# Optimization experiments

Hardware: AMD Instinct MI355X
Metric: run time of the kernel (lower is better)

The kernel has to match this reference:

```python
import jax, jax.numpy as jnp
import numpy as np

N_NODES = 100000
N_EDGES = 1600000
NODE_DIM = 64
EDGE_DIM = 32
HIDDEN = 64
LN_EPS = 1e-5


def _leaky_relu(x):
    return jnp.where(x >= 0, x, 0.1 * x)


def setup_inputs() -> dict:
    key = jax.random.key(0)
    ks = jax.random.split(key, 12)
    inp = {
        "node_features": jax.random.normal(ks[0], (N_NODES, NODE_DIM), dtype=jnp.float32),
        "edge_index": jax.random.randint(ks[1], (2, N_EDGES), 0, N_NODES, dtype=jnp.int32),
        "edge_attr": jax.random.normal(ks[2], (N_EDGES, EDGE_DIM), dtype=jnp.float32),
        "edge_weights": jax.random.uniform(ks[3], (N_EDGES,), dtype=jnp.float32),
        # message_mlp: Linear(node+edge -> hidden), LeakyReLU(0.1), Linear(hidden -> node)
        "mW1": jax.random.normal(ks[4], (NODE_DIM + EDGE_DIM, HIDDEN), dtype=jnp.float32) * 0.1,
        "mb1": jnp.zeros((HIDDEN,), dtype=jnp.float32),
        "mW2": jax.random.normal(ks[5], (HIDDEN, NODE_DIM), dtype=jnp.float32) * 0.1,
        "mb2": jnp.zeros((NODE_DIM,), dtype=jnp.float32),
        # update_mlp: Linear(2*node -> hidden), LayerNorm(hidden), LeakyReLU(0.1), Linear(hidden -> node)
        "uW1": jax.random.normal(ks[6], (2 * NODE_DIM, HIDDEN), dtype=jnp.float32) * 0.1,
        "ub1": jnp.zeros((HIDDEN,), dtype=jnp.float32),
        "ln_g": jnp.ones((HIDDEN,), dtype=jnp.float32),
        "ln_b": jnp.zeros((HIDDEN,), dtype=jnp.float32),
        "uW2": jax.random.normal(ks[7], (HIDDEN, NODE_DIM), dtype=jnp.float32) * 0.1,
        "ub2": jnp.zeros((NODE_DIM,), dtype=jnp.float32),
    }
    return inp


def reference(node_features, edge_index, edge_attr, edge_weights,
              mW1, mb1, mW2, mb2, uW1, ub1, ln_g, ln_b, uW2, ub2):
    src_idx, dst_idx = edge_index[0], edge_index[1]
    src_features = node_features[src_idx]                    # [E, node_dim] gather
    msg_input = jnp.concatenate([src_features, edge_attr], axis=-1)  # [E, node+edge]
    h = _leaky_relu(msg_input @ mW1 + mb1)                    # [E, hidden]
    messages = (h @ mW2 + mb2) * edge_weights[:, None]        # [E, node_dim]
    aggregated = jax.ops.segment_sum(messages, dst_idx, num_segments=node_features.shape[0])
    combined = jnp.concatenate([node_features, aggregated], axis=-1)  # [N, 2*node_dim]
    z = combined @ uW1 + ub1                                  # [N, hidden]
    mu = jnp.mean(z, axis=-1, keepdims=True)
    var = jnp.mean((z - mu) ** 2, axis=-1, keepdims=True)
    z = (z - mu) * jax.lax.rsqrt(var + LN_EPS) * ln_g + ln_b
    z = _leaky_relu(z)
    return z @ uW2 + ub2                                      # [N, node_dim]
```

## Files before the change

kernel.cpp:

```cpp
#include <hip/hip_runtime.h>
#include <cstdint>
#include <cstddef>

#define NN 100000
#define NE 1600000

#define QSCALE 262144.0f
#define QINV   3.814697265625e-06f

typedef __attribute__((ext_vector_type(8))) short bf16x8;
typedef __attribute__((ext_vector_type(4))) short bf16x4;
typedef __attribute__((ext_vector_type(4))) float f32x4;

#define OFF_W    0u
#define OFF_CNT  45056u
#define OFF_OFF  445056u
#define OFF_CUR  845120u
#define OFF_BS   1245120u
#define OFF_SE   1245632u
#define OFF_SD   14045632u
#define WS_NEED  20445632u

__device__ __forceinline__ short f2bf(float f) {
  uint32_t u = __builtin_bit_cast(uint32_t, f);
  u += 0x7FFFu + ((u >> 16) & 1u);
  return (short)(u >> 16);
}

__device__ __forceinline__ float lrelu(float x) { return fmaxf(x, 0.1f * x); }

__device__ __forceinline__ void atomic_add_f32(float* p, float v) {
  __hip_atomic_fetch_add(p, v, __ATOMIC_RELAXED, __HIP_MEMORY_SCOPE_AGENT);
}

__global__ void prep_kernel(const float* __restrict__ W1, const float* __restrict__ W2,
                            const float* __restrict__ uW1, const float* __restrict__ uW2,
                            short* __restrict__ ws) {
  int t = blockIdx.x * 256 + threadIdx.x;
  const int n1 = 64 * 96, n2 = 64 * 64, n3 = 64 * 128, n4 = 64 * 64;
  if (t < n1) { int c = t / 96, k = t % 96; ws[t] = f2bf(W1[k * 64 + c]); return; }
  t -= n1;
  if (t < n2) { int c = t / 64, k = t % 64; ws[n1 + t] = f2bf(W2[k * 64 + c]); return; }
  t -= n2;
  if (t < n3) { int c = t / 128, k = t % 128; ws[n1 + n2 + t] = f2bf(uW1[k * 64 + c]); return; }
  t -= n3;
  if (t < n4) { int c = t / 64, k = t % 64; ws[n1 + n2 + n3 + t] = f2bf(uW2[k * 64 + c]); return; }
}

__global__ __launch_bounds__(256) void hist_kernel(const int* __restrict__ ei,
                                                   int* __restrict__ cnt) {
  int t = blockIdx.x * 256 + threadIdx.x;
  if (t < NE) atomicAdd(&cnt[ei[NE + t]], 1);
}

__global__ __launch_bounds__(1024) void scan_block_kernel(const int* __restrict__ cnt,
                                                          int* __restrict__ off,
                                                          int* __restrict__ bs) {
  __shared__ int wsum[16];
  const int tid = threadIdx.x, lane = tid & 63, w = tid >> 6;
  const int i = blockIdx.x * 1024 + tid;
  int v = (i < NN) ? cnt[i] : 0;
  int x = v;
#pragma unroll
  for (int d = 1; d < 64; d <<= 1) { int t = __shfl_up(x, d); if (lane >= d) x += t; }
  if (lane == 63) wsum[w] = x;
  __syncthreads();
  if (w == 0) {
    int s = (lane < 16) ? wsum[lane] : 0;
#pragma unroll
    for (int d = 1; d < 16; d <<= 1) { int t = __shfl_up(s, d); if (lane >= d) s += t; }
    if (lane < 16) wsum[lane] = s;
  }
  __syncthreads();
  int incl = x + ((w > 0) ? wsum[w - 1] : 0);
  if (i < NN) off[i] = incl - v;
  if (tid == 1023) bs[blockIdx.x] = incl;
}

__global__ __launch_bounds__(1024) void scan_add_kernel(int* __restrict__ off,
                                                        const int* __restrict__ bs,
                                                        int* __restrict__ cur) {
  __shared__ int sbase;
  const int tid = threadIdx.x, cB = blockIdx.x;
  if (tid < 64) {
    int s = 0;
    if (tid < cB && tid < 98) s += bs[tid];
    int j2 = tid + 64;
    if (j2 < cB && j2 < 98) s += bs[j2];
#pragma unroll
    for (int d = 1; d < 64; d <<= 1) s += __shfl_xor(s, d);
    if (tid == 0) sbase = s;
  }
  __syncthreads();
  const int base = sbase;
  const int i = cB * 1024 + tid;
  if (i < NN) { int o = off[i] + base; off[i] = o; cur[i] = o; }
}

__global__ __launch_bounds__(256) void scatter_kernel(const int* __restrict__ ei,
                                                      int* __restrict__ cur,
                                                      int2* __restrict__ sse,
                                                      int* __restrict__ sdst) {
  int t = blockIdx.x * 256 + threadIdx.x;
  if (t >= NE) return;
  int d = ei[NE + t];
  int pos = atomicAdd(&cur[d], 1);
  sse[pos] = make_int2(ei[t], t);
  sdst[pos] = d;
}

__global__ __launch_bounds__(128) void fused_kernel(
    const float* __restrict__ nf, const float* __restrict__ ea,
    const float* __restrict__ ew,
    const int2* __restrict__ sse, const int* __restrict__ sdst,
    const int* __restrict__ off,
    const short* __restrict__ W1t, const float* __restrict__ b1,
    const short* __restrict__ W2t, const float* __restrict__ b2,
    const short* __restrict__ uW1t, const float* __restrict__ ub1,
    const float* __restrict__ gam, const float* __restrict__ bet,
    const short* __restrict__ uW2t, const float* __restrict__ ub2,
    float* __restrict__ out) {
  __shared__ __align__(16) char hbuf[2][8192];
  __shared__ int   sAgg[32 * 65];
  __shared__ int   tdstS[2][64];
  __shared__ float twS[2][64];

  const int tid = threadIdx.x;
  const int wv = tid >> 6, ln = tid & 63;
  const int c = ln & 15, g = ln >> 4;
  char* hb = hbuf[wv];
  const int nb = blockIdx.x * 32;

  for (int i = tid; i < 32 * 65; i += 128) sAgg[i] = 0;

  const int e0 = off[nb];
  const int e1 = (nb + 32 >= NN) ? NE : off[nb + 32];
  __syncthreads();

  float b1v[4][4];
#pragma unroll
  for (int m = 0; m < 4; ++m)
#pragma unroll
    for (int r = 0; r < 4; ++r) b1v[m][r] = b1[16 * m + 4 * g + r];
  float b2v[4];
#pragma unroll
  for (int n = 0; n < 4; ++n) b2v[n] = b2[16 * n + c];

  int t0 = e0 + wv * 64;
  if (t0 < e1) {
    int msx, msy, md; float mw;
    {
      int slot = t0 + ln;
      int cl = (slot < e1) ? slot : (e1 - 1);
      int2 se = sse[cl];
      msx = se.x; msy = se.y; md = sdst[cl]; mw = ew[se.y];
    }

    for (; t0 < e1; t0 += 128) {
      {
        bool val = (t0 + ln) < e1;
        tdstS[wv][ln] = val ? (md - nb) : 0;
        twS[wv][ln]   = val ? mw : 0.f;
      }
      int src[4], eid[4];
#pragma unroll
      for (int n = 0; n < 4; ++n) {
        src[n] = __shfl(msx, 16 * n + c);
        eid[n] = __shfl(msy, 16 * n + c);
      }

      int nsx = msx, nsy = msy, nd = md; float nw = mw;
      if (t0 + 128 < e1) {
        int slot = t0 + 128 + ln;
        int cl = (slot < e1) ? slot : (e1 - 1);
        int2 se = sse[cl];
        nsx = se.x; nsy = se.y; nd = sdst[cl]; nw = ew[se.y];
      }

      f32x4 acc1[4][4];
#pragma unroll
      for (int i = 0; i < 4; ++i)
#pragma unroll
        for (int j = 0; j < 4; ++j) acc1[i][j] = f32x4{0.f, 0.f, 0.f, 0.f};

#pragma unroll
      for (int ks = 0; ks < 3; ++ks) {
        bf16x8 xf[4];
#pragma unroll
        for (int n = 0; n < 4; ++n) {
          const float* p = (ks < 2) ? (nf + (size_t)src[n] * 64 + ks * 32 + g * 8)
                                    : (ea + (size_t)eid[n] * 32 + g * 8);
          float4 u = *(const float4*)p;
          float4 v = *(const float4*)(p + 4);
          bf16x8 t;
          t[0] = f2bf(u.x); t[1] = f2bf(u.y); t[2] = f2bf(u.z); t[3] = f2bf(u.w);
          t[4] = f2bf(v.x); t[5] = f2bf(v.y); t[6] = f2bf(v.z); t[7] = f2bf(v.w);
          xf[n] = t;
        }
#pragma unroll
        for (int m = 0; m < 4; ++m) {
          bf16x8 wf = *(const bf16x8*)(W1t + (size_t)(16 * m + c) * 96 + ks * 32 + g * 8);
#pragma unroll
          for (int n = 0; n < 4; ++n)
            acc1[m][n] = __builtin_amdgcn_mfma_f32_16x16x32_bf16(wf, xf[n], acc1[m][n], 0, 0, 0);
        }
      }

#pragma unroll
      for (int m = 0; m < 4; ++m) {
        const int h0 = 16 * m + 4 * g;
#pragma unroll
        for (int n = 0; n < 4; ++n) {
          const int e = 16 * n + c;
          bf16x4 pk;
#pragma unroll
          for (int r = 0; r < 4; ++r) pk[r] = f2bf(lrelu(acc1[m][n][r] + b1v[m][r]));
          const int byte = e * 128 + ((h0 * 2) ^ ((e & 7) << 4));
          *(bf16x4*)(hb + byte) = pk;
        }
      }

      f32x4 acc2[4][4];
#pragma unroll
      for (int i = 0; i < 4; ++i)
#pragma unroll
        for (int j = 0; j < 4; ++j) acc2[i][j] = f32x4{0.f, 0.f, 0.f, 0.f};
#pragma unroll
      for (int ks = 0; ks < 2; ++ks) {
        bf16x8 hf[4];
#pragma unroll
        for (int m = 0; m < 4; ++m) {
          const int e = 16 * m + c;
          const int byte = e * 128 + ((ks * 64 + g * 16) ^ ((e & 7) << 4));
          hf[m] = *(const bf16x8*)(hb + byte);
        }
#pragma unroll
        for (int n = 0; n < 4; ++n) {
          bf16x8 wf = *(const bf16x8*)(W2t + (size_t)(16 * n + c) * 64 + ks * 32 + g * 8);
#pragma unroll
          for (int m = 0; m < 4; ++m)
            acc2[m][n] = __builtin_amdgcn_mfma_f32_16x16x32_bf16(hf[m], wf, acc2[m][n], 0, 0, 0);
        }
      }

#pragma unroll
      for (int m = 0; m < 4; ++m)
#pragma unroll
        for (int r = 0; r < 4; ++r) {
          const int el = 16 * m + 4 * g + r;
          const int dl = tdstS[wv][el];
          const float w = twS[wv][el];
#pragma unroll
          for (int n = 0; n < 4; ++n)
            atomicAdd(&sAgg[dl * 65 + 16 * n + c],
                      __float2int_rn((acc2[m][n][r] + b2v[n]) * w * QSCALE));
        }

      msx = nsx; msy = nsy; md = nd; mw = nw;
    }
  }
  __syncthreads();

  const int nodeN = nb + 16 * wv + c;

  f32x4 un[4];
#pragma unroll
  for (int m = 0; m < 4; ++m) un[m] = f32x4{0.f, 0.f, 0.f, 0.f};

#pragma unroll
  for (int ks = 0; ks < 4; ++ks) {
    bf16x8 xf;
    if (ks < 2) {
      const float* p = nf + (size_t)nodeN * 64 + ks * 32 + g * 8;
      float4 u = *(const float4*)p;
      float4 v = *(const float4*)(p + 4);
      xf[0] = f2bf(u.x); xf[1] = f2bf(u.y); xf[2] = f2bf(u.z); xf[3] = f2bf(u.w);
      xf[4] = f2bf(v.x); xf[5] = f2bf(v.y); xf[6] = f2bf(v.z); xf[7] = f2bf(v.w);
    } else {
      const int* p = sAgg + (16 * wv + c) * 65 + (ks - 2) * 32 + g * 8;
#pragma unroll
      for (int j = 0; j < 8; ++j) xf[j] = f2bf((float)p[j] * QINV);
    }
#pragma unroll
    for (int m = 0; m < 4; ++m) {
      bf16x8 wf = *(const bf16x8*)(uW1t + (size_t)(16 * m + c) * 128 + ks * 32 + g * 8);
      un[m] = __builtin_amdgcn_mfma_f32_16x16x32_bf16(wf, xf, un[m], 0, 0, 0);
    }
  }

  float b1n[4][4], gn[4][4], bn[4][4];
#pragma unroll
  for (int m = 0; m < 4; ++m)
#pragma unroll
    for (int r = 0; r < 4; ++r) {
      int h = 16 * m + 4 * g + r;
      b1n[m][r] = ub1[h]; gn[m][r] = gam[h]; bn[m][r] = bet[h];
    }

  float s = 0.f;
#pragma unroll
  for (int m = 0; m < 4; ++m)
#pragma unroll
    for (int r = 0; r < 4; ++r) { un[m][r] += b1n[m][r]; s += un[m][r]; }
  s += __shfl_xor(s, 16);
  s += __shfl_xor(s, 32);
  const float mu = s * 0.015625f;
  float vs = 0.f;
#pragma unroll
  for (int m = 0; m < 4; ++m)
#pragma unroll
    for (int r = 0; r < 4; ++r) { float d = un[m][r] - mu; vs += d * d; }
  vs += __shfl_xor(vs, 16);
  vs += __shfl_xor(vs, 32);
  const float rstd = rsqrtf(vs * 0.015625f + 1e-5f);

#pragma unroll
  for (int m = 0; m < 4; ++m) {
    bf16x4 pk;
#pragma unroll
    for (int r = 0; r < 4; ++r)
      pk[r] = f2bf(lrelu((un[m][r] - mu) * rstd * gn[m][r] + bn[m][r]));
    const int byte = c * 128 + (((16 * m + 4 * g) * 2) ^ ((c & 7) << 4));
    *(bf16x4*)(hb + byte) = pk;
  }

  f32x4 ac[4];
#pragma unroll
  for (int n = 0; n < 4; ++n) ac[n] = f32x4{0.f, 0.f, 0.f, 0.f};
#pragma unroll
  for (int ks = 0; ks < 2; ++ks) {
    const int byte = c * 128 + ((ks * 64 + g * 16) ^ ((c & 7) << 4));
    bf16x8 hf = *(const bf16x8*)(hb + byte);
#pragma unroll
    for (int n = 0; n < 4; ++n) {
      bf16x8 wf = *(const bf16x8*)(uW2t + (size_t)(16 * n + c) * 64 + ks * 32 + g * 8);
      ac[n] = __builtin_amdgcn_mfma_f32_16x16x32_bf16(hf, wf, ac[n], 0, 0, 0);
    }
  }

  float b2n[4];
#pragma unroll
  for (int n = 0; n < 4; ++n) b2n[n] = ub2[16 * n + c];
#pragma unroll
  for (int r = 0; r < 4; ++r) {
    const int node = nb + 16 * wv + 4 * g + r;
    float* op = out + (size_t)node * 64 + c;
#pragma unroll
    for (int n = 0; n < 4; ++n) op[16 * n] = ac[n][r] + b2n[n];
  }
}

__global__ __launch_bounds__(256) void edge_kernel(
    const float* __restrict__ nf, const int* __restrict__ ei,
    const float* __restrict__ ea, const float* __restrict__ ew,
    const short* __restrict__ W1t, const float* __restrict__ b1,
    const short* __restrict__ W2t, const float* __restrict__ b2,
    float* __restrict__ agg) {
  __shared__ uint4 hbuf_s[4][512];
  const int tid = threadIdx.x;
  const int wv = tid >> 6, ln = tid & 63;
  const int c = ln & 15, g = ln >> 4;
  char* hb = (char*)hbuf_s[wv];
  const long base = ((long)blockIdx.x * 4 + wv) * 64;

  int eid[4], srcn[4];
#pragma unroll
  for (int n = 0; n < 4; ++n) {
    eid[n] = (int)base + 16 * n + c;
    srcn[n] = ei[eid[n]];
  }
  f32x4 acc1[4][4];
#pragma unroll
  for (int i = 0; i < 4; ++i)
#pragma unroll
    for (int j = 0; j < 4; ++j) acc1[i][j] = f32x4{0.f, 0.f, 0.f, 0.f};
#pragma unroll
  for (int ks = 0; ks < 3; ++ks) {
    bf16x8 xf[4];
#pragma unroll
    for (int n = 0; n < 4; ++n) {
      const float* p = (ks < 2) ? (nf + (size_t)srcn[n] * 64 + ks * 32 + g * 8)
                                : (ea + (size_t)eid[n] * 32 + g * 8);
      float4 u = *(const float4*)p;
      float4 v = *(const float4*)(p + 4);
      bf16x8 t;
      t[0] = f2bf(u.x); t[1] = f2bf(u.y); t[2] = f2bf(u.z); t[3] = f2bf(u.w);
      t[4] = f2bf(v.x); t[5] = f2bf(v.y); t[6] = f2bf(v.z); t[7] = f2bf(v.w);
      xf[n] = t;
    }
#pragma unroll
    for (int m = 0; m < 4; ++m) {
      bf16x8 wf = *(const bf16x8*)(W1t + (size_t)(16 * m + c) * 96 + ks * 32 + g * 8);
#pragma unroll
      for (int n = 0; n < 4; ++n)
        acc1[m][n] = __builtin_amdgcn_mfma_f32_16x16x32_bf16(wf, xf[n], acc1[m][n], 0, 0, 0);
    }
  }
  float b1v[4][4];
#pragma unroll
  for (int m = 0; m < 4; ++m)
#pragma unroll
    for (int r = 0; r < 4; ++r) b1v[m][r] = b1[16 * m + 4 * g + r];
#pragma unroll
  for (int m = 0; m < 4; ++m) {
    const int h0 = 16 * m + 4 * g;
#pragma unroll
    for (int n = 0; n < 4; ++n) {
      const int e = 16 * n + c;
      bf16x4 pk;
#pragma unroll
      for (int r = 0; r < 4; ++r) pk[r] = f2bf(lrelu(acc1[m][n][r] + b1v[m][r]));
      const int byte = e * 128 + ((h0 * 2) ^ ((e & 7) << 4));
      *(bf16x4*)(hb + byte) = pk;
    }
  }
  f32x4 acc2[4][4];
#pragma unroll
  for (int i = 0; i < 4; ++i)
#pragma unroll
    for (int j = 0; j < 4; ++j) acc2[i][j] = f32x4{0.f, 0.f, 0.f, 0.f};
#pragma unroll
  for (int ks = 0; ks < 2; ++ks) {
    bf16x8 hf[4];
#pragma unroll
    for (int m = 0; m < 4; ++m) {
      const int e = 16 * m + c;
      const int byte = e * 128 + ((ks * 64 + g * 16) ^ ((e & 7) << 4));
      hf[m] = *(const bf16x8*)(hb + byte);
    }
#pragma unroll
    for (int n = 0; n < 4; ++n) {
      bf16x8 wf = *(const bf16x8*)(W2t + (size_t)(16 * n + c) * 64 + ks * 32 + g * 8);
#pragma unroll
      for (int m = 0; m < 4; ++m)
        acc2[m][n] = __builtin_amdgcn_mfma_f32_16x16x32_bf16(hf[m], wf, acc2[m][n], 0, 0, 0);
    }
  }
  float b2v[4];
#pragma unroll
  for (int n = 0; n < 4; ++n) b2v[n] = b2[16 * n + c];
#pragma unroll
  for (int m = 0; m < 4; ++m)
#pragma unroll
    for (int r = 0; r < 4; ++r) {
      const long e = base + 16 * m + 4 * g + r;
      const float w = ew[e];
      const int dst = ei[NE + e];
      float* ab = agg + (size_t)dst * 64 + c;
#pragma unroll
      for (int n = 0; n < 4; ++n)
        atomic_add_f32(ab + 16 * n, (acc2[m][n][r] + b2v[n]) * w);
    }
}

__global__ __launch_bounds__(256) void node_kernel(
    const float* __restrict__ nf,
    const short* __restrict__ W1t, const float* __restrict__ b1,
    const float* __restrict__ gam, const float* __restrict__ bet,
    const short* __restrict__ W2t, const float* __restrict__ b2,
    float* __restrict__ io) {
  __shared__ uint4 hbuf_s[4][512];
  const int tid = threadIdx.x;
  const int wv = tid >> 6, ln = tid & 63;
  const int c = ln & 15, g = ln >> 4;
  char* hb = (char*)hbuf_s[wv];
  const long base = ((long)blockIdx.x * 4 + wv) * 64;

  int nid[4];
#pragma unroll
  for (int n = 0; n < 4; ++n) {
    long r = base + 16 * n + c;
    nid[n] = (r < NN) ? (int)r : (NN - 1);
  }
  f32x4 acc1[4][4];
#pragma unroll
  for (int i = 0; i < 4; ++i)
#pragma unroll
    for (int j = 0; j < 4; ++j) acc1[i][j] = f32x4{0.f, 0.f, 0.f, 0.f};
#pragma unroll
  for (int ks = 0; ks < 4; ++ks) {
    bf16x8 xf[4];
#pragma unroll
    for (int n = 0; n < 4; ++n) {
      const float* p = (ks < 2) ? (nf + (size_t)nid[n] * 64 + ks * 32 + g * 8)
                                : (io + (size_t)nid[n] * 64 + (ks - 2) * 32 + g * 8);
      float4 u = *(const float4*)p;
      float4 v = *(const float4*)(p + 4);
      bf16x8 t;
      t[0] = f2bf(u.x); t[1] = f2bf(u.y); t[2] = f2bf(u.z); t[3] = f2bf(u.w);
      t[4] = f2bf(v.x); t[5] = f2bf(v.y); t[6] = f2bf(v.z); t[7] = f2bf(v.w);
      xf[n] = t;
    }
#pragma unroll
    for (int m = 0; m < 4; ++m) {
      bf16x8 wf = *(const bf16x8*)(W1t + (size_t)(16 * m + c) * 128 + ks * 32 + g * 8);
#pragma unroll
      for (int n = 0; n < 4; ++n)
        acc1[m][n] = __builtin_amdgcn_mfma_f32_16x16x32_bf16(wf, xf[n], acc1[m][n], 0, 0, 0);
    }
  }
  float b1v[4][4], gv[4][4], bv[4][4];
#pragma unroll
  for (int m = 0; m < 4; ++m)
#pragma unroll
    for (int r = 0; r < 4; ++r) {
      int h = 16 * m + 4 * g + r;
      b1v[m][r] = b1[h]; gv[m][r] = gam[h]; bv[m][r] = bet[h];
    }
#pragma unroll
  for (int n = 0; n < 4; ++n) {
    float s = 0.f;
#pragma unroll
    for (int m = 0; m < 4; ++m)
#pragma unroll
      for (int r = 0; r < 4; ++r) { acc1[m][n][r] += b1v[m][r]; s += acc1[m][n][r]; }
    s += __shfl_xor(s, 16);
    s += __shfl_xor(s, 32);
    const float mu = s * 0.015625f;
    float vs = 0.f;
#pragma unroll
    for (int m = 0; m < 4; ++m)
#pragma unroll
      for (int r = 0; r < 4; ++r) { float d = acc1[m][n][r] - mu; vs += d * d; }
    vs += __shfl_xor(vs, 16);
    vs += __shfl_xor(vs, 32);
    const float rstd = rsqrtf(vs * 0.015625f + 1e-5f);
    const int e = 16 * n + c;
#pragma unroll
    for (int m = 0; m < 4; ++m) {
      bf16x4 pk;
#pragma unroll
      for (int r = 0; r < 4; ++r)
        pk[r] = f2bf(lrelu((acc1[m][n][r] - mu) * rstd * gv[m][r] + bv[m][r]));
      const int byte = e * 128 + (((16 * m + 4 * g) * 2) ^ ((e & 7) << 4));
      *(bf16x4*)(hb + byte) = pk;
    }
  }
  f32x4 acc2[4][4];
#pragma unroll
  for (int i = 0; i < 4; ++i)
#pragma unroll
    for (int j = 0; j < 4; ++j) acc2[i][j] = f32x4{0.f, 0.f, 0.f, 0.f};
#pragma unroll
  for (int ks = 0; ks < 2; ++ks) {
    bf16x8 hf[4];
#pragma unroll
    for (int m = 0; m < 4; ++m) {
      const int e = 16 * m + c;
      const int byte = e * 128 + ((ks * 64 + g * 16) ^ ((e & 7) << 4));
      hf[m] = *(const bf16x8*)(hb + byte);
    }
#pragma unroll
    for (int n = 0; n < 4; ++n) {
      bf16x8 wf = *(const bf16x8*)(W2t + (size_t)(16 * n + c) * 64 + ks * 32 + g * 8);
#pragma unroll
      for (int m = 0; m < 4; ++m)
        acc2[m][n] = __builtin_amdgcn_mfma_f32_16x16x32_bf16(hf[m], wf, acc2[m][n], 0, 0, 0);
    }
  }
  float b2v[4];
#pragma unroll
  for (int n = 0; n < 4; ++n) b2v[n] = b2[16 * n + c];
#pragma unroll
  for (int m = 0; m < 4; ++m)
#pragma unroll
    for (int r = 0; r < 4; ++r) {
      const long node = base + 16 * m + 4 * g + r;
      if (node < NN) {
        float* op = io + (size_t)node * 64 + c;
#pragma unroll
        for (int n = 0; n < 4; ++n) op[16 * n] = acc2[m][n][r] + b2v[n];
      }
    }
}

extern "C" void kernel_launch(void* const* d_in, const int* in_sizes, int n_in,
                              void* d_out, int out_size, void* d_ws, size_t ws_size,
                              hipStream_t stream) {
  const float* nf  = (const float*)d_in[0];
  const int*   ei  = (const int*)d_in[1];
  const float* ea  = (const float*)d_in[2];
  const float* ew  = (const float*)d_in[3];
  const float* mW1 = (const float*)d_in[4];
  const float* mb1 = (const float*)d_in[5];
  const float* mW2 = (const float*)d_in[6];
  const float* mb2 = (const float*)d_in[7];
  const float* uW1 = (const float*)d_in[8];
  const float* ub1 = (const float*)d_in[9];
  const float* lng = (const float*)d_in[10];
  const float* lnb = (const float*)d_in[11];
  const float* uW2 = (const float*)d_in[12];
  const float* ub2 = (const float*)d_in[13];
  float* io = (float*)d_out;
  char* ws = (char*)d_ws;

  short* Wall = (short*)(ws + OFF_W);
  prep_kernel<<<88, 256, 0, stream>>>(mW1, mW2, uW1, uW2, Wall);
  const short* W1t  = Wall;
  const short* W2t  = Wall + 64 * 96;
  const short* uW1t = Wall + 64 * 96 + 64 * 64;
  const short* uW2t = uW1t + 64 * 128;

  if (ws_size >= (size_t)WS_NEED) {
    int*  cnt  = (int*)(ws + OFF_CNT);
    int*  off  = (int*)(ws + OFF_OFF);
    int*  cur  = (int*)(ws + OFF_CUR);
    int*  bs   = (int*)(ws + OFF_BS);
    int2* sse  = (int2*)(ws + OFF_SE);
    int*  sdst = (int*)(ws + OFF_SD);

    hipMemsetAsync(cnt, 0, (size_t)NN * sizeof(int), stream);
    hist_kernel<<<NE / 256, 256, 0, stream>>>(ei, cnt);
    scan_block_kernel<<<98, 1024, 0, stream>>>(cnt, off, bs);
    scan_add_kernel<<<98, 1024, 0, stream>>>(off, bs, cur);
    scatter_kernel<<<NE / 256, 256, 0, stream>>>(ei, cur, sse, sdst);
    fused_kernel<<<NN / 32, 128, 0, stream>>>(nf, ea, ew, sse, sdst, off,
                                              W1t, mb1, W2t, mb2,
                                              uW1t, ub1, lng, lnb, uW2t, ub2, io);
  } else {
    hipMemsetAsync(d_out, 0, (size_t)NN * 64 * sizeof(float), stream);
    edge_kernel<<<NE / 256, 256, 0, stream>>>(nf, ei, ea, ew, W1t, mb1, W2t, mb2, io);
    node_kernel<<<(NN + 255) / 256, 256, 0, stream>>>(nf, uW1t, ub1, lng, lnb, uW2t, ub2, io);
  }
}
```

Baseline: 405.9 us.

## Pre-convert node features to bf16, pack dst into sorted edges, halve tiles

A new prep kernel converts node features to bf16 once, so the per-edge source gathers read half the bytes and skip conversion. The local destination index is packed into the low 5 bits of the sorted source word, which removes the separate sdst array and its store and load. Per-edge metadata now travels by shuffles instead of shared-memory staging. The edge loop handles 32 edges per half-step with smaller accumulators and launch_bounds(128,4) to raise occupancy. The costs are an extra conversion pass over all node features and more workspace; if the workspace is too small, the fp32 path is used instead.

```diff
diff --git a/kernel.cpp b/kernel.cpp
--- a/kernel.cpp
+++ b/kernel.cpp
@@ -15,11 +15,12 @@
 #define OFF_W    0u
 #define OFF_CNT  45056u
 #define OFF_OFF  445056u
-#define OFF_CUR  845120u
-#define OFF_BS   1245120u
-#define OFF_SE   1245632u
-#define OFF_SD   14045632u
-#define WS_NEED  20445632u
+#define OFF_CUR  845056u
+#define OFF_BS   1245056u
+#define OFF_SE   1245568u
+#define OFF_NFB  14045568u
+#define WS_BASE  14045568u
+#define WS_NFB   26845568u
 
 __device__ __forceinline__ short f2bf(float f) {
   uint32_t u = __builtin_bit_cast(uint32_t, f);
@@ -47,6 +48,18 @@
   if (t < n4) { int c = t / 64, k = t % 64; ws[n1 + n2 + n3 + t] = f2bf(uW2[k * 64 + c]); return; }
 }
 
+__global__ __launch_bounds__(256) void prep_nfb_kernel(const float* __restrict__ nf,
+                                                       short* __restrict__ nfb) {
+  int i = (blockIdx.x * 256 + threadIdx.x) * 8;
+  if (i >= NN * 64) return;
+  float4 u = *(const float4*)(nf + i);
+  float4 v = *(const float4*)(nf + i + 4);
+  bf16x8 t;
+  t[0] = f2bf(u.x); t[1] = f2bf(u.y); t[2] = f2bf(u.z); t[3] = f2bf(u.w);
+  t[4] = f2bf(v.x); t[5] = f2bf(v.y); t[6] = f2bf(v.z); t[7] = f2bf(v.w);
+  *(bf16x8*)(nfb + i) = t;
+}
+
 __global__ __launch_bounds__(256) void hist_kernel(const int* __restrict__ ei,
                                                    int* __restrict__ cnt) {
   int t = blockIdx.x * 256 + threadIdx.x;
@@ -99,31 +112,27 @@
 
 __global__ __launch_bounds__(256) void scatter_kernel(const int* __restrict__ ei,
                                                       int* __restrict__ cur,
-                                                      int2* __restrict__ sse,
-                                                      int* __restrict__ sdst) {
+                                                      int2* __restrict__ sse) {
   int t = blockIdx.x * 256 + threadIdx.x;
   if (t >= NE) return;
   int d = ei[NE + t];
   int pos = atomicAdd(&cur[d], 1);
-  sse[pos] = make_int2(ei[t], t);
-  sdst[pos] = d;
-}
-
-__global__ __launch_bounds__(128) void fused_kernel(
-    const float* __restrict__ nf, const float* __restrict__ ea,
-    const float* __restrict__ ew,
-    const int2* __restrict__ sse, const int* __restrict__ sdst,
-    const int* __restrict__ off,
+  sse[pos] = make_int2((ei[t] << 5) | (d & 31), t);
+}
+
+template <int NFB>
+__global__ __launch_bounds__(128, 4) void fused_kernel(
+    const float* __restrict__ nf, const short* __restrict__ nfb,
+    const float* __restrict__ ea, const float* __restrict__ ew,
+    const int2* __restrict__ sse, const int* __restrict__ off,
     const short* __restrict__ W1t, const float* __restrict__ b1,
     const short* __restrict__ W2t, const float* __restrict__ b2,
     const short* __restrict__ uW1t, const float* __restrict__ ub1,
     const float* __restrict__ gam, const float* __restrict__ bet,
     const short* __restrict__ uW2t, const float* __restrict__ ub2,
     float* __restrict__ out) {
-  __shared__ __align__(16) char hbuf[2][8192];
-  __shared__ int   sAgg[32 * 65];
-  __shared__ int   tdstS[2][64];
-  __shared__ float twS[2][64];
+  __shared__ __align__(16) char hbuf[2][4096];
+  __shared__ int sAgg[32 * 65];
 
   const int tid = threadIdx.x;
   const int wv = tid >> 6, ln = tid & 63;
@@ -148,115 +157,119 @@
 
   int t0 = e0 + wv * 64;
   if (t0 < e1) {
-    int msx, msy, md; float mw;
+    int mx, my; float mw;
     {
       int slot = t0 + ln;
       int cl = (slot < e1) ? slot : (e1 - 1);
       int2 se = sse[cl];
-      msx = se.x; msy = se.y; md = sdst[cl]; mw = ew[se.y];
+      mx = se.x; my = se.y;
+      mw = (slot < e1) ? ew[se.y] : 0.f;
     }
 
     for (; t0 < e1; t0 += 128) {
-      {
-        bool val = (t0 + ln) < e1;
-        tdstS[wv][ln] = val ? (md - nb) : 0;
-        twS[wv][ln]   = val ? mw : 0.f;
-      }
-      int src[4], eid[4];
-#pragma unroll
-      for (int n = 0; n < 4; ++n) {
-        src[n] = __shfl(msx, 16 * n + c);
-        eid[n] = __shfl(msy, 16 * n + c);
-      }
-
-      int nsx = msx, nsy = msy, nd = md; float nw = mw;
+      int nx = mx, ny = my; float nw = mw;
       if (t0 + 128 < e1) {
         int slot = t0 + 128 + ln;
         int cl = (slot < e1) ? slot : (e1 - 1);
         int2 se = sse[cl];
-        nsx = se.x; nsy = se.y; nd = sdst[cl]; nw = ew[se.y];
+        nx = se.x; ny = se.y;
+        nw = (slot < e1) ? ew[se.y] : 0.f;
       }
 
-      f32x4 acc1[4][4];
-#pragma unroll
-      for (int i = 0; i < 4; ++i)
-#pragma unroll
-        for (int j = 0; j < 4; ++j) acc1[i][j] = f32x4{0.f, 0.f, 0.f, 0.f};
-
-#pragma unroll
-      for (int ks = 0; ks < 3; ++ks) {
-        bf16x8 xf[4];
-#pragma unroll
-        for (int n = 0; n < 4; ++n) {
-          const float* p = (ks < 2) ? (nf + (size_t)src[n] * 64 + ks * 32 + g * 8)
-                                    : (ea + (size_t)eid[n] * 32 + g * 8);
-          float4 u = *(const float4*)p;
-          float4 v = *(const float4*)(p + 4);
-          bf16x8 t;
-          t[0] = f2bf(u.x); t[1] = f2bf(u.y); t[2] = f2bf(u.z); t[3] = f2bf(u.w);
-          t[4] = f2bf(v.x); t[5] = f2bf(v.y); t[6] = f2bf(v.z); t[7] = f2bf(v.w);
-          xf[n] = t;
+      for (int h = 0; h < 2; ++h) {
+        int src[2], eid[2];
+#pragma unroll
+        for (int n = 0; n < 2; ++n) {
+          int el = 32 * h + 16 * n + c;
+          src[n] = ((unsigned)__shfl(mx, el)) >> 5;
+          eid[n] = __shfl(my, el);
         }
+
+        f32x4 acc1[4][2];
+#pragma unroll
+        for (int i = 0; i < 4; ++i)
+#pragma unroll
+          for (int j = 0; j < 2; ++j) acc1[i][j] = f32x4{0.f, 0.f, 0.f, 0.f};
+
+#pragma unroll
+        for (int ks = 0; ks < 3; ++ks) {
+          bf16x8 xf[2];
+#pragma unroll
+          for (int n = 0; n < 2; ++n) {
+            if (ks < 2 && NFB) {
+              xf[n] = *(const bf16x8*)(nfb + (size_t)src[n] * 64 + ks * 32 + g * 8);
+            } else {
+              const float* p = (ks < 2) ? (nf + (size_t)src[n] * 64 + ks * 32 + g * 8)
+                                        : (ea + (size_t)eid[n] * 32 + g * 8);
+              float4 u = *(const float4*)p;
+              float4 v = *(const float4*)(p + 4);
+              bf16x8 t;
+              t[0] = f2bf(u.x); t[1] = f2bf(u.y); t[2] = f2bf(u.z); t[3] = f2bf(u.w);
+              t[4] = f2bf(v.x); t[5] = f2bf(v.y); t[6] = f2bf(v.z); t[7] = f2bf(v.w);
+              xf[n] = t;
+            }
+          }
+#pragma unroll
+          for (int m = 0; m < 4; ++m) {
+            bf16x8 wf = *(const bf16x8*)(W1t + (size_t)(16 * m + c) * 96 + ks * 32 + g * 8);
+#pragma unroll
+            for (int n = 0; n < 2; ++n)
+              acc1[m][n] = __builtin_amdgcn_mfma_f32_16x16x32_bf16(wf, xf[n], acc1[m][n], 0, 0, 0);
+          }
+        }
+
 #pragma unroll
         for (int m = 0; m < 4; ++m) {
-          bf16x8 wf = *(const bf16x8*)(W1t + (size_t)(16 * m + c) * 96 + ks * 32 + g * 8);
-#pragma unroll
-          for (int n = 0; n < 4; ++n)
-            acc1[m][n] = __builtin_amdgcn_mfma_f32_16x16x32_bf16(wf, xf[n], acc1[m][n], 0, 0, 0);
+          const int h0 = 16 * m + 4 * g;
+#pragma unroll
+          for (int n = 0; n < 2; ++n) {
+            const int e = 16 * n + c;
+            bf16x4 pk;
+#pragma unroll
+            for (int r = 0; r < 4; ++r) pk[r] = f2bf(lrelu(acc1[m][n][r] + b1v[m][r]));
+            const int byte = e * 128 + ((h0 * 2) ^ ((e & 7) << 4));
+            *(bf16x4*)(hb + byte) = pk;
+          }
         }
+
+        f32x4 acc2[2][4];
+#pragma unroll
+        for (int i = 0; i < 2; ++i)
+#pragma unroll
+          for (int j = 0; j < 4; ++j) acc2[i][j] = f32x4{0.f, 0.f, 0.f, 0.f};
+#pragma unroll
+        for (int ks = 0; ks < 2; ++ks) {
+          bf16x8 hf[2];
+#pragma unroll
+          for (int m = 0; m < 2; ++m) {
+            const int e = 16 * m + c;
+            const int byte = e * 128 + ((ks * 64 + g * 16) ^ ((e & 7) << 4));
+            hf[m] = *(const bf16x8*)(hb + byte);
+          }
+#pragma unroll
+          for (int n = 0; n < 4; ++n) {
+            bf16x8 wf = *(const bf16x8*)(W2t + (size_t)(16 * n + c) * 64 + ks * 32 + g * 8);
+#pragma unroll
+            for (int m = 0; m < 2; ++m)
+              acc2[m][n] = __builtin_amdgcn_mfma_f32_16x16x32_bf16(hf[m], wf, acc2[m][n], 0, 0, 0);
+          }
+        }
+
+#pragma unroll
+        for (int m = 0; m < 2; ++m)
+#pragma unroll
+          for (int r = 0; r < 4; ++r) {
+            const int el = 32 * h + 16 * m + 4 * g + r;
+            const int dl = __shfl(mx, el) & 31;
+            const float w = __shfl(mw, el);
+#pragma unroll
+            for (int n = 0; n < 4; ++n)
+              atomicAdd(&sAgg[dl * 65 + 16 * n + c],
+                        __float2int_rn((acc2[m][n][r] + b2v[n]) * w * QSCALE));
+          }
       }
 
-#pragma unroll
-      for (int m = 0; m < 4; ++m) {
-        const int h0 = 16 * m + 4 * g;
-#pragma unroll
-        for (int n = 0; n < 4; ++n) {
-          const int e = 16 * n + c;
-          bf16x4 pk;
-#pragma unroll
-          for (int r = 0; r < 4; ++r) pk[r] = f2bf(lrelu(acc1[m][n][r] + b1v[m][r]));
-          const int byte = e * 128 + ((h0 * 2) ^ ((e & 7) << 4));
-          *(bf16x4*)(hb + byte) = pk;
-        }
-      }
-
-      f32x4 acc2[4][4];
-#pragma unroll
-      for (int i = 0; i < 4; ++i)
-#pragma unroll
-        for (int j = 0; j < 4; ++j) acc2[i][j] = f32x4{0.f, 0.f, 0.f, 0.f};
-#pragma unroll
-      for (int ks = 0; ks < 2; ++ks) {
-        bf16x8 hf[4];
-#pragma unroll
-        for (int m = 0; m < 4; ++m) {
-          const int e = 16 * m + c;
-          const int byte = e * 128 + ((ks * 64 + g * 16) ^ ((e & 7) << 4));
-          hf[m] = *(const bf16x8*)(hb + byte);
-        }
-#pragma unroll
-        for (int n = 0; n < 4; ++n) {
-          bf16x8 wf = *(const bf16x8*)(W2t + (size_t)(16 * n + c) * 64 + ks * 32 + g * 8);
-#pragma unroll
-          for (int m = 0; m < 4; ++m)
-            acc2[m][n] = __builtin_amdgcn_mfma_f32_16x16x32_bf16(hf[m], wf, acc2[m][n], 0, 0, 0);
-        }
-      }
-
-#pragma unroll
-      for (int m = 0; m < 4; ++m)
-#pragma unroll
-        for (int r = 0; r < 4; ++r) {
-          const int el = 16 * m + 4 * g + r;
-          const int dl = tdstS[wv][el];
-          const float w = twS[wv][el];
-#pragma unroll
-          for (int n = 0; n < 4; ++n)
-            atomicAdd(&sAgg[dl * 65 + 16 * n + c],
-                      __float2int_rn((acc2[m][n][r] + b2v[n]) * w * QSCALE));
-        }
-
-      msx = nsx; msy = nsy; md = nd; mw = nw;
+      mx = nx; my = ny; mw = nw;
     }
   }
   __syncthreads();
@@ -271,11 +284,15 @@
   for (int ks = 0; ks < 4; ++ks) {
     bf16x8 xf;
     if (ks < 2) {
-      const float* p = nf + (size_t)nodeN * 64 + ks * 32 + g * 8;
-      float4 u = *(const float4*)p;
-      float4 v = *(const float4*)(p + 4);
-      xf[0] = f2bf(u.x); xf[1] = f2bf(u.y); xf[2] = f2bf(u.z); xf[3] = f2bf(u.w);
-      xf[4] = f2bf(v.x); xf[5] = f2bf(v.y); xf[6] = f2bf(v.z); xf[7] = f2bf(v.w);
+      if (NFB) {
+        xf = *(const bf16x8*)(nfb + (size_t)nodeN * 64 + ks * 32 + g * 8);
+      } else {
+        const float* p = nf + (size_t)nodeN * 64 + ks * 32 + g * 8;
+        float4 u = *(const float4*)p;
+        float4 v = *(const float4*)(p + 4);
+        xf[0] = f2bf(u.x); xf[1] = f2bf(u.y); xf[2] = f2bf(u.z); xf[3] = f2bf(u.w);
+        xf[4] = f2bf(v.x); xf[5] = f2bf(v.y); xf[6] = f2bf(v.z); xf[7] = f2bf(v.w);
+      }
     } else {
       const int* p = sAgg + (16 * wv + c) * 65 + (ks - 2) * 32 + g * 8;
 #pragma unroll
@@ -601,22 +618,30 @@
   const short* uW1t = Wall + 64 * 96 + 64 * 64;
   const short* uW2t = uW1t + 64 * 128;
 
-  if (ws_size >= (size_t)WS_NEED) {
-    int*  cnt  = (int*)(ws + OFF_CNT);
-    int*  off  = (int*)(ws + OFF_OFF);
-    int*  cur  = (int*)(ws + OFF_CUR);
-    int*  bs   = (int*)(ws + OFF_BS);
-    int2* sse  = (int2*)(ws + OFF_SE);
-    int*  sdst = (int*)(ws + OFF_SD);
-
+  if (ws_size >= (size_t)WS_BASE) {
+    int*  cnt = (int*)(ws + OFF_CNT);
+    int*  off = (int*)(ws + OFF_OFF);
+    int*  cur = (int*)(ws + OFF_CUR);
+    int*  bs  = (int*)(ws + OFF_BS);
+    int2* sse = (int2*)(ws + OFF_SE);
+    short* nfb = (short*)(ws + OFF_NFB);
+    const bool use_nfb = ws_size >= (size_t)WS_NFB;
+
+    if (use_nfb)
+      prep_nfb_kernel<<<(NN * 64 / 8 + 255) / 256, 256, 0, stream>>>(nf, nfb);
     hipMemsetAsync(cnt, 0, (size_t)NN * sizeof(int), stream);
     hist_kernel<<<NE / 256, 256, 0, stream>>>(ei, cnt);
     scan_block_kernel<<<98, 1024, 0, stream>>>(cnt, off, bs);
     scan_add_kernel<<<98, 1024, 0, stream>>>(off, bs, cur);
-    scatter_kernel<<<NE / 256, 256, 0, stream>>>(ei, cur, sse, sdst);
-    fused_kernel<<<NN / 32, 128, 0, stream>>>(nf, ea, ew, sse, sdst, off,
-                                              W1t, mb1, W2t, mb2,
-                                              uW1t, ub1, lng, lnb, uW2t, ub2, io);
+    scatter_kernel<<<NE / 256, 256, 0, stream>>>(ei, cur, sse);
+    if (use_nfb)
+      fused_kernel<1><<<NN / 32, 128, 0, stream>>>(nf, nfb, ea, ew, sse, off,
+                                                   W1t, mb1, W2t, mb2,
+                                                   uW1t, ub1, lng, lnb, uW2t, ub2, io);
+    else
+      fused_kernel<0><<<NN / 32, 128, 0, stream>>>(nf, nfb, ea, ew, sse, off,
+                                                   W1t, mb1, W2t, mb2,
+                                                   uW1t, ub1, lng, lnb, uW2t, ub2, io);
   } else {
     hipMemsetAsync(d_out, 0, (size_t)NN * 64 * sizeof(float), stream);
     edge_kernel<<<NE / 256, 256, 0, stream>>>(nf, ei, ea, ew, W1t, mb1, W2t, mb2, io);
```

After: 541.8 us. +33.5%, slower.
